# Performance work log

Hardware: AMD Instinct MI355X
Metric: run time of the kernel (lower is better)

## Reference

```python
import jax, jax.numpy as jnp
import numpy as np

B, S, D, H = 4, 2048, 1024, 16
DK = D // H

def setup_inputs() -> dict:
    key = jax.random.key(0)
    ks = jax.random.split(key, 5)
    scale = 1.0 / np.sqrt(D)
    return {
        "x": jax.random.normal(ks[0], (B, S, D), dtype=jnp.float32),
        "Wq": jax.random.normal(ks[1], (H, D, DK), dtype=jnp.float32) * scale,
        "Wk": jax.random.normal(ks[2], (H, D, DK), dtype=jnp.float32) * scale,
        "Wv": jax.random.normal(ks[3], (H, D, DK), dtype=jnp.float32) * scale,
        "Wo": jax.random.normal(ks[4], (D, D), dtype=jnp.float32) * scale,
    }

def reference(x, Wq, Wk, Wv, Wo):
    # x: [B,S,D]; Wq/Wk/Wv: [H,D,DK] (stacked per-head Linear weights); Wo: [D,D]
    seq = x.shape[-2]
    q = jnp.einsum('bsd,hdk->bhsk', x, Wq)
    k = jnp.einsum('bsd,hdk->bhsk', x, Wk)
    v = jnp.einsum('bsd,hdk->bhsk', x, Wv)
    dk = q.shape[-1]
    scores = jnp.einsum('bhqk,bhsk->bhqs', q, k) / jnp.sqrt(jnp.asarray(dk, x.dtype))
    # causal mask: mask out strictly-future positions (triu, diagonal=1)
    causal = jnp.tril(jnp.ones((seq, seq), dtype=bool))  # True = keep
    scores = jnp.where(causal, scores, -jnp.inf)
    probs = jax.nn.softmax(scores, axis=-1)  # attn_pdrop = 0.0 -> dropout is identity
    attn = jnp.einsum('bhqs,bhsk->bhqk', probs, v)
    # concat heads: [B,S,H*DK]
    concat = attn.transpose(0, 2, 1, 3).reshape(x.shape[0], seq, -1)
    # output_proj: nn.Linear(D, D, bias=False) -> y = concat @ Wo.T
    return jnp.einsum('bsd,ed->bse', concat, Wo)
```

## Files before the change

### kernel.cpp

```cpp
#include <hip/hip_runtime.h>
#include <hip/hip_bf16.h>

#define B_ 4
#define S_ 2048
#define D_ 1024
#define H_ 16
#define DK_ 64

typedef __attribute__((ext_vector_type(8))) short bf16x8;
typedef __attribute__((ext_vector_type(4))) float f32x4;
typedef __attribute__((ext_vector_type(4))) unsigned int u32x4;

__device__ __forceinline__ unsigned short f2bf(float f) {
    unsigned int u = __float_as_uint(f);
    u += 0x7FFFu + ((u >> 16) & 1u);
    return (unsigned short)(u >> 16);
}

__device__ __forceinline__ unsigned int cvtpk_bf16(float lo, float hi) {
    unsigned int r;
    asm("v_cvt_pk_bf16_f32 %0, %1, %2" : "=v"(r) : "v"(lo), "v"(hi));
    return r;
}

#define BAR() do { __builtin_amdgcn_s_barrier(); asm volatile("" ::: "memory"); } while (0)

__global__ void cvt_kernel(const float* __restrict__ src, unsigned short* __restrict__ dst) {
    int i = (blockIdx.x * 256 + threadIdx.x) * 8;
    float4 f0 = *(const float4*)&src[i];
    float4 f1 = *(const float4*)&src[i + 4];
    unsigned short t[8] __attribute__((aligned(16))) = {
        f2bf(f0.x), f2bf(f0.y), f2bf(f0.z), f2bf(f0.w),
        f2bf(f1.x), f2bf(f1.y), f2bf(f1.z), f2bf(f1.w)};
    *(u32x4*)&dst[i] = *(const u32x4*)t;
}

__global__ void prepack_kernel(const float* __restrict__ Wq,
                               const float* __restrict__ Wk,
                               const float* __restrict__ Wv,
                               unsigned short* __restrict__ Wt) {
    __shared__ unsigned short Ts[64 * 65];
    int h = blockIdx.x, w3 = blockIdx.y, t = blockIdx.z;
    const float* src = (w3 == 0 ? Wq : (w3 == 1 ? Wk : Wv)) + h * D_ * DK_ + t * 64 * DK_;
    unsigned short* dst = Wt + (w3 * H_ + h) * DK_ * D_ + t * 64;
    const float wscale = (w3 == 0) ? 0.18033688011112042f : 1.0f;
    int tid = threadIdx.x;
    for (int rep = 0; rep < 16; ++rep) {
        int idx = rep * 256 + tid;
        int dl = idx >> 6, k = idx & 63;
        Ts[k * 65 + dl] = f2bf(src[dl * 64 + k] * wscale);
    }
    __syncthreads();
    for (int rep = 0; rep < 16; ++rep) {
        int idx = rep * 256 + tid;
        int kl = idx >> 6, dl = idx & 63;
        dst[kl * D_ + dl] = Ts[kl * 65 + dl];
    }
}

__global__ __launch_bounds__(256) void prep_kernel(const float* __restrict__ x,
                                                   const float* __restrict__ Wq,
                                                   const float* __restrict__ Wk,
                                                   const float* __restrict__ Wv,
                                                   const float* __restrict__ Wo,
                                                   unsigned short* __restrict__ xbf,
                                                   unsigned short* __restrict__ Wt,
                                                   unsigned short* __restrict__ Wobf) {
    __shared__ unsigned short Ts[64 * 65];
    const int bid = blockIdx.x;
    const int tid = threadIdx.x;
    if (bid < 4096 + 512) {
        const bool isx = bid < 4096;
        const float* src = isx ? x : Wo;
        unsigned short* dst = isx ? xbf : Wobf;
        int i = ((isx ? bid : bid - 4096) * 256 + tid) * 8;
        float4 f0 = *(const float4*)&src[i];
        float4 f1 = *(const float4*)&src[i + 4];
        unsigned short t[8] __attribute__((aligned(16))) = {
            f2bf(f0.x), f2bf(f0.y), f2bf(f0.z), f2bf(f0.w),
            f2bf(f1.x), f2bf(f1.y), f2bf(f1.z), f2bf(f1.w)};
        *(u32x4*)&dst[i] = *(const u32x4*)t;
    } else {
        const int pid = bid - 4608;
        const int h = pid & 15, w3 = (pid >> 4) % 3, t = pid / 48;
        const float* src = (w3 == 0 ? Wq : (w3 == 1 ? Wk : Wv)) + h * D_ * DK_ + t * 64 * DK_;
        unsigned short* dst = Wt + (w3 * H_ + h) * DK_ * D_ + t * 64;
        const float wscale = (w3 == 0) ? 0.18033688011112042f : 1.0f;
        for (int rep = 0; rep < 16; ++rep) {
            int idx = rep * 256 + tid;
            int dl = idx >> 6, k = idx & 63;
            Ts[k * 65 + dl] = f2bf(src[dl * 64 + k] * wscale);
        }
        __syncthreads();
        for (int rep = 0; rep < 16; ++rep) {
            int idx = rep * 256 + tid;
            int kl = idx >> 6, dl = idx & 63;
            dst[kl * D_ + dl] = Ts[kl * 65 + dl];
        }
    }
}

__device__ __forceinline__ void gload16(const unsigned short* gp, unsigned short* lp) {
    __builtin_amdgcn_global_load_lds((const __attribute__((address_space(1))) unsigned int*)gp,
                                     (__attribute__((address_space(3))) unsigned int*)lp,
                                     16, 0, 0);
}

__device__ __forceinline__ void stageA_half(const unsigned short* __restrict__ g,
                                            unsigned short* lds_base, int wv, int lane, int ldg) {
    int r = wv * 8 + (lane >> 3);
    int gc = (lane & 7) ^ ((lane >> 3) & 7);
    gload16(g + r * ldg + gc * 8, lds_base + (wv * 8) * 64);
}

__device__ __forceinline__ void stageB_half(const unsigned short* __restrict__ g,
                                            unsigned short* lds_base, int wv, int lane, int ldg) {
#pragma unroll
    for (int L = 0; L < 2; ++L) {
        int rbase = wv * 16 + L * 8;
        int r = rbase + (lane >> 3);
        int gc = (lane & 7) ^ ((lane >> 3) & 7);
        gload16(g + r * ldg + gc * 8, lds_base + rbase * 64);
    }
}

__device__ __forceinline__ void stage64_async(const unsigned short* __restrict__ g,
                                              unsigned short* lds_base, int wv, int lane, int ldg) {
#pragma unroll
    for (int it = 0; it < 2; ++it) {
        int rbase = wv * 16 + it * 8;
        int r = rbase + (lane >> 3);
        int gc = (lane & 7) ^ ((lane >> 3) & 7);
        gload16(g + r * ldg + gc * 8, lds_base + rbase * 64);
    }
}

template <int MH, int NH>
__device__ __forceinline__ void phase_mfma(const unsigned short* Asl, const unsigned short* Bsl,
                                           int db, int wm, int wn, int l15, int q4,
                                           f32x4 (&acc)[2][2][2][2]) {
    bf16x8 af[2][2], bf[2][2];
#pragma unroll
    for (int kk = 0; kk < 2; ++kk) {
        const int sw = ((kk * 4 + q4) ^ (l15 & 7)) * 8;
#pragma unroll
        for (int m4 = 0; m4 < 2; ++m4)
            af[m4][kk] = *(const bf16x8*)&Asl[(db + MH) * 4096 + (wm * 32 + m4 * 16 + l15) * 64 + sw];
#pragma unroll
        for (int n2 = 0; n2 < 2; ++n2)
            bf[n2][kk] = *(const bf16x8*)&Bsl[(db + NH) * 8192 + (wn * 32 + n2 * 16 + l15) * 64 + sw];
    }
    __builtin_amdgcn_s_setprio(1);
#pragma unroll
    for (int kk = 0; kk < 2; ++kk)
#pragma unroll
        for (int m4 = 0; m4 < 2; ++m4)
#pragma unroll
            for (int n2 = 0; n2 < 2; ++n2)
                acc[MH][NH][m4][n2] =
                    __builtin_amdgcn_mfma_f32_16x16x32_bf16(af[m4][kk], bf[n2][kk], acc[MH][NH][m4][n2], 0, 0, 0);
    __builtin_amdgcn_s_setprio(0);
}

template <bool QKV_OUT>
__global__ __launch_bounds__(512) void gemm256_kernel(const unsigned short* __restrict__ A,
                                                      const unsigned short* __restrict__ Bt,
                                                      void* __restrict__ Out,
                                                      unsigned short* __restrict__ VtOut) {
    __shared__ __align__(16) unsigned short lds[49152];
    unsigned short* Asl = lds;
    unsigned short* Bsl = lds + 16384;

    const int tid = threadIdx.x;
    const int wv = tid >> 6, lane = tid & 63, l15 = lane & 15, q4 = lane >> 4;
    const int wm = wv >> 2, wn = wv & 3;

    const int nwg = gridDim.x * gridDim.y;
    const int bid = blockIdx.x + blockIdx.y * gridDim.x;
    const int swz = (bid & 7) * (nwg >> 3) + (bid >> 3);
    const int bx = swz % gridDim.x, by = swz / gridDim.x;
    const int r0 = bx * 128, c0 = by * 256;

    const unsigned short* Ab = A + r0 * D_;
    const unsigned short* Bb = Bt + c0 * D_;

    f32x4 acc[2][2][2][2] = {};

    stageA_half(Ab, Asl, wv, lane, D_);
    stageB_half(Bb, Bsl, wv, lane, D_);
    stageB_half(Bb + 128 * D_, Bsl + 8192, wv, lane, D_);

    for (int j = 0; j < 16; ++j) {
        const int db = (j & 1) * 2;
        const int ndb = ((j + 1) & 1) * 2;
        const bool nx = (j + 1 < 16);

        stageA_half(Ab + 64 * D_ + j * 64, Asl + (db + 1) * 4096, wv, lane, D_);
        asm volatile("s_waitcnt vmcnt(3)" ::: "memory");
        BAR();
        phase_mfma<0, 0>(Asl, Bsl, db, wm, wn, l15, q4, acc);

        if (nx) {
            stageA_half(Ab + (j + 1) * 64, Asl + (ndb + 0) * 4096, wv, lane, D_);
            asm volatile("s_waitcnt vmcnt(2)" ::: "memory");
        } else {
            asm volatile("s_waitcnt vmcnt(1)" ::: "memory");
        }
        BAR();
        phase_mfma<0, 1>(Asl, Bsl, db, wm, wn, l15, q4, acc);

        if (nx) {
            stageB_half(Bb + (j + 1) * 64, Bsl + (ndb + 0) * 8192, wv, lane, D_);
            asm volatile("s_waitcnt vmcnt(3)" ::: "memory");
        } else {
            asm volatile("s_waitcnt vmcnt(0)" ::: "memory");
        }
        BAR();
        phase_mfma<1, 1>(Asl, Bsl, db, wm, wn, l15, q4, acc);

        if (nx) stageB_half(Bb + 128 * D_ + (j + 1) * 64, Bsl + (ndb + 1) * 8192, wv, lane, D_);
        BAR();
        phase_mfma<1, 0>(Asl, Bsl, db, wm, wn, l15, q4, acc);
    }

    __syncthreads();

    if (QKV_OUT && c0 >= 2 * D_) {
        const int b = r0 >> 11, s0 = r0 & (S_ - 1);
#pragma unroll
        for (int nh = 0; nh < 2; ++nh) {
#pragma unroll
            for (int mh = 0; mh < 2; ++mh)
#pragma unroll
                for (int m4 = 0; m4 < 2; ++m4)
#pragma unroll
                    for (int n2 = 0; n2 < 2; ++n2)
#pragma unroll
                        for (int rr = 0; rr < 4; ++rr) {
                            int cl = wn * 32 + n2 * 16 + l15;
                            int rl = mh * 64 + wm * 32 + m4 * 16 + q4 * 4 + rr;
                            lds[cl * 128 + (rl ^ ((cl & 7) * 8))] = f2bf(acc[mh][nh][m4][n2][rr]);
                        }
            __syncthreads();
#pragma unroll
            for (int rep = 0; rep < 4; ++rep) {
                int idx = rep * 512 + tid;
                int col = idx >> 4, ch = idx & 15;
                u32x4 v = *(const u32x4*)&lds[col * 128 + ((ch * 8) ^ ((col & 7) * 8))];
                int gcol = c0 + nh * 128 + col;
                int vrow = b * 1024 + (gcol & 1023);
                *(u32x4*)&VtOut[vrow * S_ + s0 + ch * 8] = v;
            }
            __syncthreads();
        }
    } else {
#pragma unroll
        for (int mh = 0; mh < 2; ++mh)
#pragma unroll
            for (int nh = 0; nh < 2; ++nh)
#pragma unroll
                for (int m4 = 0; m4 < 2; ++m4)
#pragma unroll
                    for (int n2 = 0; n2 < 2; ++n2)
#pragma unroll
                        for (int rr = 0; rr < 4; ++rr) {
                            int grow = r0 + mh * 64 + wm * 32 + m4 * 16 + q4 * 4 + rr;
                            int gcol = c0 + nh * 128 + wn * 32 + n2 * 16 + l15;
                            if (QKV_OUT) {
                                int b = grow >> 11, s = grow & (S_ - 1);
                                int w3 = gcol >> 10, h = (gcol >> 6) & 15, dk = gcol & 63;
                                ((unsigned short*)Out)[(((w3 * B_ + b) * H_ + h) * S_ + s) * DK_ + dk] =
                                    f2bf(acc[mh][nh][m4][n2][rr]);
                            } else {
                                ((float*)Out)[grow * D_ + gcol] = acc[mh][nh][m4][n2][rr];
                            }
                        }
    }
}

__global__ __launch_bounds__(256) void attn_kernel(const unsigned short* __restrict__ qkv,
                                                   unsigned short* __restrict__ concat) {
    static const int J[16] = {15, 13, 11, 9, 0, 2, 4, 6, 14, 12, 10, 8, 1, 3, 5, 7};
    const int bh = blockIdx.x;
    const int b = bh >> 4, h = bh & 15;
    const int j = J[blockIdx.y];
    const int q0 = j * 128;
    const int nk = 2 * j + 2;

    const unsigned short* Qp = qkv + ((0 * B_ + b) * H_ + h) * S_ * DK_;
    const unsigned short* Kp = qkv + ((1 * B_ + b) * H_ + h) * S_ * DK_;
    const unsigned short* Vt = qkv + 2 * B_ * H_ * S_ * DK_ + (b * H_ + h) * DK_ * S_;

    __shared__ __align__(16) unsigned short Kb[2][64 * 64];
    __shared__ __align__(16) unsigned short Vb[2][64 * 64];

    const int tid = threadIdx.x;
    const int wv = tid >> 6, lane = tid & 63, l15 = lane & 15, q4 = lane >> 4;

    stage64_async(Kp, Kb[0], wv, lane, DK_);
    stage64_async(Vt, Vb[0], wv, lane, S_);

    bf16x8 aq[2][2];
#pragma unroll
    for (int rt = 0; rt < 2; ++rt)
#pragma unroll
        for (int kk = 0; kk < 2; ++kk)
            aq[rt][kk] = *(const bf16x8*)&Qp[(q0 + wv * 32 + rt * 16 + l15) * DK_ + kk * 32 + q4 * 8];

    f32x4 o[2][4] = {};
    float l_[2] = {0.0f, 0.0f};

    __syncthreads();

    for (int t = 0; t < nk; ++t) {
        const int k0 = t * 64;
        if (t + 1 < nk) {
            stage64_async(Kp + (k0 + 64) * DK_, Kb[(t + 1) & 1], wv, lane, DK_);
            stage64_async(Vt + (k0 + 64), Vb[(t + 1) & 1], wv, lane, S_);
        }
        const unsigned short* Kt = Kb[t & 1];
        const unsigned short* Vtt = Vb[t & 1];

        if ((t + 1 < nk) || (wv >= 2)) {
            f32x4 sa[2][4] = {};
            __builtin_amdgcn_s_setprio(1);
#pragma unroll
            for (int kk = 0; kk < 2; ++kk) {
                const int sw = ((kk * 4 + q4) ^ (l15 & 7)) * 8;
#pragma unroll
                for (int ct = 0; ct < 4; ++ct) {
                    bf16x8 bk = *(const bf16x8*)&Kt[(ct * 16 + l15) * 64 + sw];
                    sa[0][ct] = __builtin_amdgcn_mfma_f32_16x16x32_bf16(bk, aq[0][kk], sa[0][ct], 0, 0, 0);
                    sa[1][ct] = __builtin_amdgcn_mfma_f32_16x16x32_bf16(bk, aq[1][kk], sa[1][ct], 0, 0, 0);
                }
            }
            __builtin_amdgcn_s_setprio(0);

            if (t < nk - 2) {
#pragma unroll
                for (int rt = 0; rt < 2; ++rt)
#pragma unroll
                    for (int ct = 0; ct < 4; ++ct)
#pragma unroll
                        for (int r = 0; r < 4; ++r)
                            sa[rt][ct][r] = __builtin_amdgcn_exp2f(sa[rt][ct][r]);
            } else {
                const int kb = k0 + q4 * 4;
#pragma unroll
                for (int rt = 0; rt < 2; ++rt) {
                    const int qrow = q0 + wv * 32 + rt * 16 + l15;
#pragma unroll
                    for (int ct = 0; ct < 4; ++ct)
#pragma unroll
                        for (int r = 0; r < 4; ++r) {
                            float e = __builtin_amdgcn_exp2f(sa[rt][ct][r]);
                            sa[rt][ct][r] = (kb + ct * 16 + r <= qrow) ? e : 0.0f;
                        }
                }
            }

#pragma unroll
            for (int rt = 0; rt < 2; ++rt)
#pragma unroll
                for (int ct = 0; ct < 4; ++ct)
                    l_[rt] += (sa[rt][ct][0] + sa[rt][ct][1]) + (sa[rt][ct][2] + sa[rt][ct][3]);

            bf16x8 F[2][2];
#pragma unroll
            for (int rt = 0; rt < 2; ++rt)
#pragma unroll
                for (int kk = 0; kk < 2; ++kk) {
                    u32x4 w;
#pragma unroll
                    for (int u = 0; u < 2; ++u) {
                        unsigned int a = cvtpk_bf16(sa[rt][2 * kk][2 * u], sa[rt][2 * kk][2 * u + 1]);
                        unsigned int c = cvtpk_bf16(sa[rt][2 * kk + 1][2 * u], sa[rt][2 * kk + 1][2 * u + 1]);
                        asm("v_permlane32_swap_b32 %0, %1" : "+v"(a), "+v"(c));
                        asm("v_permlane16_swap_b32 %0, %1" : "+v"(a), "+v"(c));
                        w[u] = a;
                        w[2 + u] = c;
                    }
                    F[rt][kk] = *(const bf16x8*)&w;
                }

            __builtin_amdgcn_s_setprio(1);
#pragma unroll
            for (int kk = 0; kk < 2; ++kk) {
                const int sw = ((kk * 4 + q4) ^ (l15 & 7)) * 8;
#pragma unroll
                for (int cd = 0; cd < 4; ++cd) {
                    bf16x8 bv = *(const bf16x8*)&Vtt[(cd * 16 + l15) * 64 + sw];
                    o[0][cd] = __builtin_amdgcn_mfma_f32_16x16x32_bf16(F[0][kk], bv, o[0][cd], 0, 0, 0);
                    o[1][cd] = __builtin_amdgcn_mfma_f32_16x16x32_bf16(F[1][kk], bv, o[1][cd], 0, 0, 0);
                }
            }
            __builtin_amdgcn_s_setprio(0);
        }
        __syncthreads();
    }

#pragma unroll
    for (int rt = 0; rt < 2; ++rt) {
        float lr = l_[rt];
        lr += __shfl_xor(lr, 16);
        lr += __shfl_xor(lr, 32);
#pragma unroll
        for (int r = 0; r < 4; ++r) {
            float lfull = __shfl(lr, (lane & 48) | (q4 * 4 + r));
            float inv = 1.0f / fmaxf(lfull, 1.0e-37f);
            int row = q0 + wv * 32 + rt * 16 + q4 * 4 + r;
#pragma unroll
            for (int cd = 0; cd < 4; ++cd) {
                int col = h * DK_ + cd * 16 + l15;
                concat[(b * S_ + row) * D_ + col] = f2bf(o[rt][cd][r] * inv);
            }
        }
    }
}

extern "C" void kernel_launch(void* const* d_in, const int* in_sizes, int n_in,
                              void* d_out, int out_size, void* d_ws, size_t ws_size,
                              hipStream_t stream) {
    const float* x  = (const float*)d_in[0];
    const float* Wq = (const float*)d_in[1];
    const float* Wk = (const float*)d_in[2];
    const float* Wv = (const float*)d_in[3];
    const float* Wo = (const float*)d_in[4];

    unsigned short* qkv    = (unsigned short*)d_ws;
    unsigned short* Wt     = qkv + 3 * B_ * H_ * S_ * DK_;
    unsigned short* xbf    = Wt + 3 * H_ * DK_ * D_;
    unsigned short* concat = xbf;
    unsigned short* VtOut  = qkv + 2 * B_ * H_ * S_ * DK_;

    const size_t need_shorts = (size_t)3 * B_ * H_ * S_ * DK_ + 3 * H_ * DK_ * D_ + B_ * S_ * D_ + D_ * D_;
    const bool sep = ws_size >= need_shorts * sizeof(unsigned short);

    if (sep) {
        unsigned short* Wobf = xbf + B_ * S_ * D_;
        prep_kernel<<<4096 + 512 + 768, 256, 0, stream>>>(x, Wq, Wk, Wv, Wo, xbf, Wt, Wobf);
        gemm256_kernel<true><<<dim3(64, 12), 512, 0, stream>>>(xbf, Wt, qkv, VtOut);
        attn_kernel<<<dim3(64, 16), 256, 0, stream>>>(qkv, concat);
        gemm256_kernel<false><<<dim3(64, 4), 512, 0, stream>>>(concat, Wobf, d_out, nullptr);
    } else {
        unsigned short* Wobf = Wt;
        cvt_kernel<<<B_ * S_ * D_ / 2048, 256, 0, stream>>>(x, xbf);
        prepack_kernel<<<dim3(H_, 3, 16), 256, 0, stream>>>(Wq, Wk, Wv, Wt);
        gemm256_kernel<true><<<dim3(64, 12), 512, 0, stream>>>(xbf, Wt, qkv, VtOut);
        cvt_kernel<<<D_ * D_ / 2048, 256, 0, stream>>>(Wo, Wobf);
        attn_kernel<<<dim3(64, 16), 256, 0, stream>>>(qkv, concat);
        gemm256_kernel<false><<<dim3(64, 4), 512, 0, stream>>>(concat, Wobf, d_out, nullptr);
    }
}
```

Measured before the change: 262.5 us.

## Enlarge GEMM tiles to 256x256 with four-phase double-buffered pipeline

The GEMM block tile grows from 128x256 to 256x256, with each wave computing 8x4 MFMA fragments and interleaved row/column assignment. The K-loop is reorganised into four phases that reuse A and B fragments held in registers across phases while the next tile's halves are staged asynchronously. The goal is higher arithmetic intensity and fewer global loads per FLOP. In exchange it uses more LDS (128KB) and many more accumulator registers, and halves the grid (384 and 128 blocks on 256 CUs), which can leave CUs underused, especially for the output projection.

```diff
diff --git a/kernel.cpp b/kernel.cpp
--- a/kernel.cpp
+++ b/kernel.cpp
@@ -106,21 +106,14 @@
                                      16, 0, 0);
 }
 
-__device__ __forceinline__ void stageA_half(const unsigned short* __restrict__ g,
-                                            unsigned short* lds_base, int wv, int lane, int ldg) {
-    int r = wv * 8 + (lane >> 3);
-    int gc = (lane & 7) ^ ((lane >> 3) & 7);
-    gload16(g + r * ldg + gc * 8, lds_base + (wv * 8) * 64);
-}
-
-__device__ __forceinline__ void stageB_half(const unsigned short* __restrict__ g,
-                                            unsigned short* lds_base, int wv, int lane, int ldg) {
+__device__ __forceinline__ void stage_half(const unsigned short* __restrict__ g,
+                                           unsigned short* slot, int h, int wv, int lane, int ldg) {
 #pragma unroll
     for (int L = 0; L < 2; ++L) {
-        int rbase = wv * 16 + L * 8;
+        int rbase = h * 128 + L * 64 + wv * 8;
         int r = rbase + (lane >> 3);
         int gc = (lane & 7) ^ ((lane >> 3) & 7);
-        gload16(g + r * ldg + gc * 8, lds_base + rbase * 64);
+        gload16(g + r * ldg + gc * 8, slot + rbase * 64);
     }
 }
 
@@ -135,42 +128,12 @@
     }
 }
 
-template <int MH, int NH>
-__device__ __forceinline__ void phase_mfma(const unsigned short* Asl, const unsigned short* Bsl,
-                                           int db, int wm, int wn, int l15, int q4,
-                                           f32x4 (&acc)[2][2][2][2]) {
-    bf16x8 af[2][2], bf[2][2];
-#pragma unroll
-    for (int kk = 0; kk < 2; ++kk) {
-        const int sw = ((kk * 4 + q4) ^ (l15 & 7)) * 8;
-#pragma unroll
-        for (int m4 = 0; m4 < 2; ++m4)
-            af[m4][kk] = *(const bf16x8*)&Asl[(db + MH) * 4096 + (wm * 32 + m4 * 16 + l15) * 64 + sw];
-#pragma unroll
-        for (int n2 = 0; n2 < 2; ++n2)
-            bf[n2][kk] = *(const bf16x8*)&Bsl[(db + NH) * 8192 + (wn * 32 + n2 * 16 + l15) * 64 + sw];
-    }
-    __builtin_amdgcn_s_setprio(1);
-#pragma unroll
-    for (int kk = 0; kk < 2; ++kk)
-#pragma unroll
-        for (int m4 = 0; m4 < 2; ++m4)
-#pragma unroll
-            for (int n2 = 0; n2 < 2; ++n2)
-                acc[MH][NH][m4][n2] =
-                    __builtin_amdgcn_mfma_f32_16x16x32_bf16(af[m4][kk], bf[n2][kk], acc[MH][NH][m4][n2], 0, 0, 0);
-    __builtin_amdgcn_s_setprio(0);
-}
-
 template <bool QKV_OUT>
-__global__ __launch_bounds__(512) void gemm256_kernel(const unsigned short* __restrict__ A,
-                                                      const unsigned short* __restrict__ Bt,
-                                                      void* __restrict__ Out,
-                                                      unsigned short* __restrict__ VtOut) {
-    __shared__ __align__(16) unsigned short lds[49152];
-    unsigned short* Asl = lds;
-    unsigned short* Bsl = lds + 16384;
-
+__global__ __launch_bounds__(512, 2) void gemm256_kernel(const unsigned short* __restrict__ A,
+                                                         const unsigned short* __restrict__ Bt,
+                                                         void* __restrict__ Out,
+                                                         unsigned short* __restrict__ VtOut) {
+    __shared__ __align__(16) unsigned short lds[65536];
     const int tid = threadIdx.x;
     const int wv = tid >> 6, lane = tid & 63, l15 = lane & 15, q4 = lane >> 4;
     const int wm = wv >> 2, wn = wv & 3;
@@ -179,48 +142,113 @@
     const int bid = blockIdx.x + blockIdx.y * gridDim.x;
     const int swz = (bid & 7) * (nwg >> 3) + (bid >> 3);
     const int bx = swz % gridDim.x, by = swz / gridDim.x;
-    const int r0 = bx * 128, c0 = by * 256;
+    const int r0 = bx * 256, c0 = by * 256;
 
     const unsigned short* Ab = A + r0 * D_;
     const unsigned short* Bb = Bt + c0 * D_;
 
-    f32x4 acc[2][2][2][2] = {};
-
-    stageA_half(Ab, Asl, wv, lane, D_);
-    stageB_half(Bb, Bsl, wv, lane, D_);
-    stageB_half(Bb + 128 * D_, Bsl + 8192, wv, lane, D_);
+    f32x4 acc[8][4] = {};
+
+    stage_half(Ab, lds, 0, wv, lane, D_);
+    stage_half(Bb, lds + 32768, 0, wv, lane, D_);
+    stage_half(Bb, lds + 32768, 1, wv, lane, D_);
+    stage_half(Ab, lds, 1, wv, lane, D_);
 
     for (int j = 0; j < 16; ++j) {
-        const int db = (j & 1) * 2;
-        const int ndb = ((j + 1) & 1) * 2;
         const bool nx = (j + 1 < 16);
-
-        stageA_half(Ab + 64 * D_ + j * 64, Asl + (db + 1) * 4096, wv, lane, D_);
-        asm volatile("s_waitcnt vmcnt(3)" ::: "memory");
+        unsigned short* Ad = lds + (j & 1) * 16384;
+        unsigned short* Bd = lds + 32768 + (j & 1) * 16384;
+        unsigned short* An = lds + ((j + 1) & 1) * 16384;
+        unsigned short* Bn = lds + 32768 + ((j + 1) & 1) * 16384;
+
+        bf16x8 af[4][2], bfA[2][2], bfB[2][2];
+
+        if (nx) {
+            stage_half(Ab + (j + 1) * 64, An, 0, wv, lane, D_);
+            asm volatile("s_waitcnt vmcnt(6)" ::: "memory");
+        } else {
+            asm volatile("s_waitcnt vmcnt(4)" ::: "memory");
+        }
         BAR();
-        phase_mfma<0, 0>(Asl, Bsl, db, wm, wn, l15, q4, acc);
+#pragma unroll
+        for (int kk = 0; kk < 2; ++kk) {
+            const int sw = ((kk * 4 + q4) ^ (l15 & 7)) * 8;
+#pragma unroll
+            for (int i = 0; i < 4; ++i)
+                af[i][kk] = *(const bf16x8*)&Ad[(i * 32 + wm * 16 + l15) * 64 + sw];
+#pragma unroll
+            for (int jf = 0; jf < 2; ++jf)
+                bfA[jf][kk] = *(const bf16x8*)&Bd[(jf * 64 + wn * 16 + l15) * 64 + sw];
+        }
+        __builtin_amdgcn_s_setprio(1);
+#pragma unroll
+        for (int kk = 0; kk < 2; ++kk)
+#pragma unroll
+            for (int i = 0; i < 4; ++i)
+#pragma unroll
+                for (int jf = 0; jf < 2; ++jf)
+                    acc[i][jf] = __builtin_amdgcn_mfma_f32_16x16x32_bf16(af[i][kk], bfA[jf][kk], acc[i][jf], 0, 0, 0);
+        __builtin_amdgcn_s_setprio(0);
 
         if (nx) {
-            stageA_half(Ab + (j + 1) * 64, Asl + (ndb + 0) * 4096, wv, lane, D_);
+            stage_half(Bb + (j + 1) * 64, Bn, 0, wv, lane, D_);
+            asm volatile("s_waitcnt vmcnt(6)" ::: "memory");
+        } else {
             asm volatile("s_waitcnt vmcnt(2)" ::: "memory");
-        } else {
-            asm volatile("s_waitcnt vmcnt(1)" ::: "memory");
         }
         BAR();
-        phase_mfma<0, 1>(Asl, Bsl, db, wm, wn, l15, q4, acc);
+#pragma unroll
+        for (int kk = 0; kk < 2; ++kk) {
+            const int sw = ((kk * 4 + q4) ^ (l15 & 7)) * 8;
+#pragma unroll
+            for (int jf = 0; jf < 2; ++jf)
+                bfB[jf][kk] = *(const bf16x8*)&Bd[((2 + jf) * 64 + wn * 16 + l15) * 64 + sw];
+        }
+        __builtin_amdgcn_s_setprio(1);
+#pragma unroll
+        for (int kk = 0; kk < 2; ++kk)
+#pragma unroll
+            for (int i = 0; i < 4; ++i)
+#pragma unroll
+                for (int jf = 0; jf < 2; ++jf)
+                    acc[i][2 + jf] = __builtin_amdgcn_mfma_f32_16x16x32_bf16(af[i][kk], bfB[jf][kk], acc[i][2 + jf], 0, 0, 0);
+        __builtin_amdgcn_s_setprio(0);
 
         if (nx) {
-            stageB_half(Bb + (j + 1) * 64, Bsl + (ndb + 0) * 8192, wv, lane, D_);
-            asm volatile("s_waitcnt vmcnt(3)" ::: "memory");
+            stage_half(Bb + (j + 1) * 64, Bn, 1, wv, lane, D_);
+            asm volatile("s_waitcnt vmcnt(6)" ::: "memory");
         } else {
             asm volatile("s_waitcnt vmcnt(0)" ::: "memory");
         }
         BAR();
-        phase_mfma<1, 1>(Asl, Bsl, db, wm, wn, l15, q4, acc);
-
-        if (nx) stageB_half(Bb + 128 * D_ + (j + 1) * 64, Bsl + (ndb + 1) * 8192, wv, lane, D_);
+#pragma unroll
+        for (int kk = 0; kk < 2; ++kk) {
+            const int sw = ((kk * 4 + q4) ^ (l15 & 7)) * 8;
+#pragma unroll
+            for (int i = 0; i < 4; ++i)
+                af[i][kk] = *(const bf16x8*)&Ad[(128 + i * 32 + wm * 16 + l15) * 64 + sw];
+        }
+        __builtin_amdgcn_s_setprio(1);
+#pragma unroll
+        for (int kk = 0; kk < 2; ++kk)
+#pragma unroll
+            for (int i = 0; i < 4; ++i)
+#pragma unroll
+                for (int jf = 0; jf < 2; ++jf)
+                    acc[4 + i][2 + jf] = __builtin_amdgcn_mfma_f32_16x16x32_bf16(af[i][kk], bfB[jf][kk], acc[4 + i][2 + jf], 0, 0, 0);
+        __builtin_amdgcn_s_setprio(0);
+
+        if (nx) stage_half(Ab + (j + 1) * 64, An, 1, wv, lane, D_);
         BAR();
-        phase_mfma<1, 0>(Asl, Bsl, db, wm, wn, l15, q4, acc);
+        __builtin_amdgcn_s_setprio(1);
+#pragma unroll
+        for (int kk = 0; kk < 2; ++kk)
+#pragma unroll
+            for (int i = 0; i < 4; ++i)
+#pragma unroll
+                for (int jf = 0; jf < 2; ++jf)
+                    acc[4 + i][jf] = __builtin_amdgcn_mfma_f32_16x16x32_bf16(af[i][kk], bfA[jf][kk], acc[4 + i][jf], 0, 0, 0);
+        __builtin_amdgcn_s_setprio(0);
     }
 
     __syncthreads();
@@ -228,53 +256,47 @@
     if (QKV_OUT && c0 >= 2 * D_) {
         const int b = r0 >> 11, s0 = r0 & (S_ - 1);
 #pragma unroll
-        for (int nh = 0; nh < 2; ++nh) {
-#pragma unroll
-            for (int mh = 0; mh < 2; ++mh)
-#pragma unroll
-                for (int m4 = 0; m4 < 2; ++m4)
-#pragma unroll
-                    for (int n2 = 0; n2 < 2; ++n2)
-#pragma unroll
-                        for (int rr = 0; rr < 4; ++rr) {
-                            int cl = wn * 32 + n2 * 16 + l15;
-                            int rl = mh * 64 + wm * 32 + m4 * 16 + q4 * 4 + rr;
-                            lds[cl * 128 + (rl ^ ((cl & 7) * 8))] = f2bf(acc[mh][nh][m4][n2][rr]);
+        for (int mh = 0; mh < 2; ++mh)
+#pragma unroll
+            for (int ii = 0; ii < 4; ++ii)
+#pragma unroll
+                for (int jf = 0; jf < 4; ++jf)
+#pragma unroll
+                    for (int rr = 0; rr < 4; ++rr) {
+                        int cl = jf * 64 + wn * 16 + l15;
+                        int rl = mh * 128 + ii * 32 + wm * 16 + q4 * 4 + rr;
+                        lds[cl * 256 + (rl ^ ((cl & 7) * 8))] = f2bf(acc[mh * 4 + ii][jf][rr]);
+                    }
+        __syncthreads();
+#pragma unroll
+        for (int rep = 0; rep < 16; ++rep) {
+            int idx = rep * 512 + tid;
+            int col = idx >> 5, ch = idx & 31;
+            u32x4 v = *(const u32x4*)&lds[col * 256 + ((ch * 8) ^ ((col & 7) * 8))];
+            int gcol = c0 + col;
+            int vrow = b * 1024 + (gcol & 1023);
+            *(u32x4*)&VtOut[vrow * S_ + s0 + ch * 8] = v;
+        }
+    } else {
+#pragma unroll
+        for (int mh = 0; mh < 2; ++mh)
+#pragma unroll
+            for (int ii = 0; ii < 4; ++ii)
+#pragma unroll
+                for (int jf = 0; jf < 4; ++jf)
+#pragma unroll
+                    for (int rr = 0; rr < 4; ++rr) {
+                        int grow = r0 + mh * 128 + ii * 32 + wm * 16 + q4 * 4 + rr;
+                        int gcol = c0 + jf * 64 + wn * 16 + l15;
+                        if (QKV_OUT) {
+                            int bb = grow >> 11, s = grow & (S_ - 1);
+                            int w3 = gcol >> 10, h = (gcol >> 6) & 15, dk = gcol & 63;
+                            ((unsigned short*)Out)[(((w3 * B_ + bb) * H_ + h) * S_ + s) * DK_ + dk] =
+                                f2bf(acc[mh * 4 + ii][jf][rr]);
+                        } else {
+                            ((float*)Out)[grow * D_ + gcol] = acc[mh * 4 + ii][jf][rr];
                         }
-            __syncthreads();
-#pragma unroll
-            for (int rep = 0; rep < 4; ++rep) {
-                int idx = rep * 512 + tid;
-                int col = idx >> 4, ch = idx & 15;
-                u32x4 v = *(const u32x4*)&lds[col * 128 + ((ch * 8) ^ ((col & 7) * 8))];
-                int gcol = c0 + nh * 128 + col;
-                int vrow = b * 1024 + (gcol & 1023);
-                *(u32x4*)&VtOut[vrow * S_ + s0 + ch * 8] = v;
-            }
-            __syncthreads();
-        }
-    } else {
-#pragma unroll
-        for (int mh = 0; mh < 2; ++mh)
-#pragma unroll
-            for (int nh = 0; nh < 2; ++nh)
-#pragma unroll
-                for (int m4 = 0; m4 < 2; ++m4)
-#pragma unroll
-                    for (int n2 = 0; n2 < 2; ++n2)
-#pragma unroll
-                        for (int rr = 0; rr < 4; ++rr) {
-                            int grow = r0 + mh * 64 + wm * 32 + m4 * 16 + q4 * 4 + rr;
-                            int gcol = c0 + nh * 128 + wn * 32 + n2 * 16 + l15;
-                            if (QKV_OUT) {
-                                int b = grow >> 11, s = grow & (S_ - 1);
-                                int w3 = gcol >> 10, h = (gcol >> 6) & 15, dk = gcol & 63;
-                                ((unsigned short*)Out)[(((w3 * B_ + b) * H_ + h) * S_ + s) * DK_ + dk] =
-                                    f2bf(acc[mh][nh][m4][n2][rr]);
-                            } else {
-                                ((float*)Out)[grow * D_ + gcol] = acc[mh][nh][m4][n2][rr];
-                            }
-                        }
+                    }
     }
 }
 
@@ -439,16 +461,16 @@
     if (sep) {
         unsigned short* Wobf = xbf + B_ * S_ * D_;
         prep_kernel<<<4096 + 512 + 768, 256, 0, stream>>>(x, Wq, Wk, Wv, Wo, xbf, Wt, Wobf);
-        gemm256_kernel<true><<<dim3(64, 12), 512, 0, stream>>>(xbf, Wt, qkv, VtOut);
+        gemm256_kernel<true><<<dim3(32, 12), 512, 0, stream>>>(xbf, Wt, qkv, VtOut);
         attn_kernel<<<dim3(64, 16), 256, 0, stream>>>(qkv, concat);
-        gemm256_kernel<false><<<dim3(64, 4), 512, 0, stream>>>(concat, Wobf, d_out, nullptr);
+        gemm256_kernel<false><<<dim3(32, 4), 512, 0, stream>>>(concat, Wobf, d_out, nullptr);
     } else {
         unsigned short* Wobf = Wt;
         cvt_kernel<<<B_ * S_ * D_ / 2048, 256, 0, stream>>>(x, xbf);
         prepack_kernel<<<dim3(H_, 3, 16), 256, 0, stream>>>(Wq, Wk, Wv, Wt);
-        gemm256_kernel<true><<<dim3(64, 12), 512, 0, stream>>>(xbf, Wt, qkv, VtOut);
+        gemm256_kernel<true><<<dim3(32, 12), 512, 0, stream>>>(xbf, Wt, qkv, VtOut);
         cvt_kernel<<<D_ * D_ / 2048, 256, 0, stream>>>(Wo, Wobf);
         attn_kernel<<<dim3(64, 16), 256, 0, stream>>>(qkv, concat);
-        gemm256_kernel<false><<<dim3(64, 4), 512, 0, stream>>>(concat, Wobf, d_out, nullptr);
-    }
-}
+        gemm256_kernel<false><<<dim3(32, 4), 512, 0, stream>>>(concat, Wobf, d_out, nullptr);
+    }
+}
```

After: 248.6 us. -5.3%, faster.
